# Kernel optimization log

Measured on AMD Instinct MI355X. Metric: run time of the kernel, lower is better.

## Reference

```python
import jax, jax.numpy as jnp
import numpy as np

FIRE_RATE = 0.5  # from init_kwargs
TOTAL_C = 16     # hidden_channels + 1


def _perception_filters(C, dtype):
    # Faithful to reg_perception_filters (including the sobel_x entries as written).
    identity = jnp.array([[0.0, 0.0, 0.0], [0.0, 1.0, 0.0], [0.0, 0.0, 0.0]], dtype=dtype)
    sobel_x = jnp.array([[1.0, 0.0, 1.0], [2.0, 0.0, -2.0], [1.0, 0.0, -1.0]], dtype=dtype) / 8.0
    sobel_y = jnp.array([[1.0, 2.0, 1.0], [0.0, 0.0, 0.0], [-1.0, -2.0, -1.0]], dtype=dtype) / 8.0
    f = jnp.stack([identity, sobel_x, sobel_y])[:, None, :, :]  # [3,1,3,3]
    # Grouped depthwise conv: each input channel -> 3 outputs, ordered
    # [ch0_id, ch0_sx, ch0_sy, ch1_id, ...] matching the torch per-channel cat.
    return jnp.tile(f, (C, 1, 1, 1))  # [3C,1,3,3]


def setup_inputs() -> dict:
    key = jax.random.key(0)
    k1, k2, k3, k4, k5, k6 = jax.random.split(key, 6)
    B, C, H, W = 32, TOTAL_C, 256, 256
    P = 3 * C  # perception channels = 48
    return {
        "grid": jax.random.normal(k1, (B, C, H, W), dtype=jnp.float32),
        "noise": jax.random.normal(k2, (B, 1, H, W), dtype=jnp.float32),
        "w1": jax.random.normal(k3, (128, P), dtype=jnp.float32) * 0.05,
        "b1": jax.random.normal(k4, (128,), dtype=jnp.float32) * 0.05,
        "w2": jax.random.normal(k5, (C, 128), dtype=jnp.float32) * 0.05,
        "b2": jax.random.normal(k6, (C,), dtype=jnp.float32) * 0.05,
    }


def reference(grid, noise, w1, b1, w2, b2):
    B, C, H, W = grid.shape
    filt = _perception_filters(C, grid.dtype)  # [3C,1,3,3]
    # Per-channel identity/sobel stencil as one grouped depthwise conv.
    perception = jax.lax.conv_general_dilated(
        grid, filt, window_strides=(1, 1), padding="SAME",
        dimension_numbers=("NCHW", "OIHW", "NCHW"), feature_group_count=C,
    )  # [B,3C,H,W]
    # update_net: 1x1 conv -> ReLU -> 1x1 conv (expressed as channel GEMMs)
    h = jax.nn.relu(jnp.einsum("oc,bchw->bohw", w1, perception) + b1[None, :, None, None])
    update = jnp.einsum("oc,bchw->bohw", w2, h) + b2[None, :, None, None]
    # stochastic mask: (randn < fire_rate), broadcast over channels
    mask = (noise < FIRE_RATE).astype(grid.dtype)
    return jnp.clip(grid + update * mask, -2.0, 2.0)
```

## Files before the change

kernel.cpp:

```cpp
#include <hip/hip_runtime.h>

#define NC   16
#define NP   48
#define NH   128
#define HDIM 256
#define WDIM 256
#define HW   (HDIM*WDIM)

#define PSTR  56
#define W1STR 56
#define W2STR 136
#define HSTR  136

typedef __attribute__((ext_vector_type(8))) short short8;
typedef __attribute__((ext_vector_type(4))) float f32x4;

__device__ __forceinline__ short f2bf(float f) {
    unsigned u = __float_as_uint(f);
    u += 0x7FFFu + ((u >> 16) & 1u);
    return (short)(u >> 16);
}

__global__ __launch_bounds__(256, 3) void nca_mfma_kernel(
    const float* __restrict__ grid,
    const float* __restrict__ noise,
    const float* __restrict__ w1,
    const float* __restrict__ b1,
    const float* __restrict__ w2,
    const float* __restrict__ b2,
    float* __restrict__ out)
{
    __shared__ short sP[HDIM * PSTR + 8];
    __shared__ union {
        struct { short w1[NH * W1STR + 8]; short w2[NC * W2STR]; } s;
        short H[4][16 * HSTR];
    } sU;

    const int tid = threadIdx.x;
    const int b = blockIdx.x >> 8;
    const int y = blockIdx.x & 255;

    {
        const int x = tid;
        const bool ym = (y > 0), yp = (y < HDIM - 1);
        const bool xm = (x > 0), xp = (x < WDIM - 1);
        const int xl = xm ? x - 1 : 0;
        const int xr = xp ? x + 1 : x;
        const size_t base = (size_t)b * NC * HW + (size_t)y * WDIM;

        float p[NP];
        #pragma unroll
        for (int c = 0; c < NC; ++c) {
            const float* rowM = grid + base + (size_t)c * HW;
            const float* rowT = rowM + (ym ? -WDIM : 0);
            const float* rowB = rowM + (yp ?  WDIM : 0);

            float tl0 = rowT[xl], tm0 = rowT[x], tr0 = rowT[xr];
            float ml0 = rowM[xl], mm  = rowM[x], mr0 = rowM[xr];
            float bl0 = rowB[xl], bm0 = rowB[x], br0 = rowB[xr];

            float tl = (ym && xm) ? tl0 : 0.f;
            float tm = ym         ? tm0 : 0.f;
            float tr = (ym && xp) ? tr0 : 0.f;
            float ml = xm         ? ml0 : 0.f;
            float mr = xp         ? mr0 : 0.f;
            float bl = (yp && xm) ? bl0 : 0.f;
            float bm = yp         ? bm0 : 0.f;
            float br = (yp && xp) ? br0 : 0.f;

            p[3*c]     = mm;
            p[3*c + 1] = (tl + tr + 2.f*ml - 2.f*mr + bl - br) * 0.125f;
            p[3*c + 2] = (tl + 2.f*tm + tr - bl - 2.f*bm - br) * 0.125f;
        }
        short* pw = &sP[x * PSTR];
        #pragma unroll
        for (int i = 0; i < 6; ++i) {
            short8 v;
            #pragma unroll
            for (int j = 0; j < 8; ++j) v[j] = f2bf(p[8*i + j]);
            *(short8*)&pw[8*i] = v;
        }
        short8 z = {};
        *(short8*)&pw[48] = z;
        if (tid == 0) *(short8*)&sP[HDIM * PSTR] = z;
    }

    {
        const int o = tid >> 1, half = tid & 1;
        const float* src = w1 + o * NP + half * 24;
        short* dst = &sU.s.w1[o * W1STR + half * 24];
        #pragma unroll
        for (int i = 0; i < 3; ++i) {
            short8 v;
            #pragma unroll
            for (int j = 0; j < 8; ++j) v[j] = f2bf(src[8*i + j]);
            *(short8*)&dst[8*i] = v;
        }
        if (half) { short8 z = {}; *(short8*)&sU.s.w1[o * W1STR + 48] = z; }
    }
    {
        const int j = tid >> 4, seg = tid & 15;
        const float* src = w2 + j * NH + seg * 8;
        short8 v;
        #pragma unroll
        for (int k = 0; k < 8; ++k) v[k] = f2bf(src[k]);
        *(short8*)&sU.s.w2[j * W2STR + seg * 8] = v;
    }
    __syncthreads();

    const int wv   = tid >> 6;
    const int lane = tid & 63;
    const int q    = lane >> 4;
    const int l15  = lane & 15;

    short8 w1f[8][2];
    #pragma unroll
    for (int n = 0; n < 8; ++n) {
        #pragma unroll
        for (int t = 0; t < 2; ++t) {
            const int kb = 32*t + 8*q;
            short8 v = *(const short8*)&sU.s.w1[(16*n + l15) * W1STR + kb];
            if (kb >= NP) { short8 z = {}; v = z; }
            w1f[n][t] = v;
        }
    }
    short8 w2f[4];
    #pragma unroll
    for (int t = 0; t < 4; ++t) {
        short8 v;
        #pragma unroll
        for (int jj = 0; jj < 8; ++jj) v[jj] = sU.s.w2[l15 * W2STR + jj*16 + 4*t + q];
        w2f[t] = v;
    }
    float b1v[8];
    #pragma unroll
    for (int n = 0; n < 8; ++n) b1v[n] = b1[16*n + l15];
    const float b2v = b2[l15];

    __syncthreads();

    short* Hb = sU.H[wv];
    #pragma unroll
    for (int mt = 0; mt < 4; ++mt) {
        const int px0 = (wv * 4 + mt) * 16;
        const short* pr = &sP[(px0 + l15) * PSTR];
        const short8 a0 = *(const short8*)&pr[8*q];
        short8 a1 = *(const short8*)&pr[32 + 8*q];
        if (q == 3) { short8 z = {}; a1 = z; }

        f32x4 acc[8];
        #pragma unroll
        for (int n = 0; n < 8; ++n) { f32x4 t4 = {b1v[n], b1v[n], b1v[n], b1v[n]}; acc[n] = t4; }
        #pragma unroll
        for (int n = 0; n < 8; ++n) {
            acc[n] = __builtin_amdgcn_mfma_f32_16x16x32_bf16(a0, w1f[n][0], acc[n], 0, 0, 0);
            acc[n] = __builtin_amdgcn_mfma_f32_16x16x32_bf16(a1, w1f[n][1], acc[n], 0, 0, 0);
        }
        #pragma unroll
        for (int r = 0; r < 4; ++r) {
            short8 hv;
            #pragma unroll
            for (int n = 0; n < 8; ++n) hv[n] = f2bf(fmaxf(acc[n][r], 0.f));
            *(short8*)&Hb[(q*4 + r) * HSTR + l15 * 8] = hv;
        }
        f32x4 acc2 = {b2v, b2v, b2v, b2v};
        #pragma unroll
        for (int t = 0; t < 4; ++t) {
            const short8 af = *(const short8*)&Hb[l15 * HSTR + 32*t + 8*q];
            acc2 = __builtin_amdgcn_mfma_f32_16x16x32_bf16(af, w2f[t], acc2, 0, 0, 0);
        }
        const int px = px0 + 4*q;
        const size_t gi = (size_t)b * NC * HW + (size_t)l15 * HW + (size_t)y * WDIM + px;
        const float4 g  = *(const float4*)&grid[gi];
        const float4 nz = *(const float4*)&noise[(size_t)b * HW + (size_t)y * WDIM + px];
        float4 o;
        o.x = fminf(fmaxf(g.x + acc2[0] * (nz.x < 0.5f ? 1.f : 0.f), -2.f), 2.f);
        o.y = fminf(fmaxf(g.y + acc2[1] * (nz.y < 0.5f ? 1.f : 0.f), -2.f), 2.f);
        o.z = fminf(fmaxf(g.z + acc2[2] * (nz.z < 0.5f ? 1.f : 0.f), -2.f), 2.f);
        o.w = fminf(fmaxf(g.w + acc2[3] * (nz.w < 0.5f ? 1.f : 0.f), -2.f), 2.f);
        *(float4*)&out[gi] = o;
    }
}

extern "C" void kernel_launch(void* const* d_in, const int* in_sizes, int n_in,
                              void* d_out, int out_size, void* d_ws, size_t ws_size,
                              hipStream_t stream) {
    const float* grid  = (const float*)d_in[0];
    const float* noise = (const float*)d_in[1];
    const float* w1    = (const float*)d_in[2];
    const float* b1    = (const float*)d_in[3];
    const float* w2    = (const float*)d_in[4];
    const float* b2    = (const float*)d_in[5];
    float* out = (float*)d_out;

    dim3 g(32 * 256);
    nca_mfma_kernel<<<g, 256, 0, stream>>>(grid, noise, w1, b1, w2, b2, out);
}
```

Before: 412.9 us.

## Stage stencil rows through LDS, keep W1 fragments in LDS, raise occupancy

Stencil inputs are now loaded cooperatively as three float4 rows per channel into shared memory, double-stepped with barriers, instead of nine scalar global loads per thread per channel. W1 fragments are kept pre-swizzled in LDS and read per MFMA rather than held in registers. The perception and H buffers now share one LDS region, and launch bounds are raised to 4 blocks per SM. Float-to-bf16 conversion uses the packed hardware instruction. The per-channel loop now has two barriers per channel, 32 in total, which adds synchronization overhead in exchange for fewer registers and less redundant global traffic.

```diff
diff --git a/kernel.cpp b/kernel.cpp
--- a/kernel.cpp
+++ b/kernel.cpp
@@ -7,21 +7,21 @@
 #define WDIM 256
 #define HW   (HDIM*WDIM)
 
-#define PSTR  56
-#define W1STR 56
+#define PSTR  48
+#define HSTR  136
 #define W2STR 136
-#define HSTR  136
 
 typedef __attribute__((ext_vector_type(8))) short short8;
 typedef __attribute__((ext_vector_type(4))) float f32x4;
-
-__device__ __forceinline__ short f2bf(float f) {
-    unsigned u = __float_as_uint(f);
-    u += 0x7FFFu + ((u >> 16) & 1u);
-    return (short)(u >> 16);
+typedef __attribute__((ext_vector_type(4))) int   int4v;
+
+__device__ __forceinline__ unsigned cvt_pk(float lo, float hi) {
+    unsigned r;
+    asm("v_cvt_pk_bf16_f32 %0, %1, %2" : "=v"(r) : "v"(lo), "v"(hi));
+    return r;
 }
 
-__global__ __launch_bounds__(256, 3) void nca_mfma_kernel(
+__global__ __launch_bounds__(256, 4) void nca_mfma_kernel(
     const float* __restrict__ grid,
     const float* __restrict__ noise,
     const float* __restrict__ w1,
@@ -30,106 +30,51 @@
     const float* __restrict__ b2,
     float* __restrict__ out)
 {
-    __shared__ short sP[HDIM * PSTR + 8];
-    __shared__ union {
-        struct { short w1[NH * W1STR + 8]; short w2[NC * W2STR]; } s;
-        short H[4][16 * HSTR];
-    } sU;
-
-    const int tid = threadIdx.x;
-    const int b = blockIdx.x >> 8;
-    const int y = blockIdx.x & 255;
-
-    {
-        const int x = tid;
-        const bool ym = (y > 0), yp = (y < HDIM - 1);
-        const bool xm = (x > 0), xp = (x < WDIM - 1);
-        const int xl = xm ? x - 1 : 0;
-        const int xr = xp ? x + 1 : x;
-        const size_t base = (size_t)b * NC * HW + (size_t)y * WDIM;
-
-        float p[NP];
-        #pragma unroll
-        for (int c = 0; c < NC; ++c) {
-            const float* rowM = grid + base + (size_t)c * HW;
-            const float* rowT = rowM + (ym ? -WDIM : 0);
-            const float* rowB = rowM + (yp ?  WDIM : 0);
-
-            float tl0 = rowT[xl], tm0 = rowT[x], tr0 = rowT[xr];
-            float ml0 = rowM[xl], mm  = rowM[x], mr0 = rowM[xr];
-            float bl0 = rowB[xl], bm0 = rowB[x], br0 = rowB[xr];
-
-            float tl = (ym && xm) ? tl0 : 0.f;
-            float tm = ym         ? tm0 : 0.f;
-            float tr = (ym && xp) ? tr0 : 0.f;
-            float ml = xm         ? ml0 : 0.f;
-            float mr = xp         ? mr0 : 0.f;
-            float bl = (yp && xm) ? bl0 : 0.f;
-            float bm = yp         ? bm0 : 0.f;
-            float br = (yp && xp) ? br0 : 0.f;
-
-            p[3*c]     = mm;
-            p[3*c + 1] = (tl + tr + 2.f*ml - 2.f*mr + bl - br) * 0.125f;
-            p[3*c + 2] = (tl + 2.f*tm + tr - bl - 2.f*bm - br) * 0.125f;
-        }
-        short* pw = &sP[x * PSTR];
-        #pragma unroll
-        for (int i = 0; i < 6; ++i) {
-            short8 v;
-            #pragma unroll
-            for (int j = 0; j < 8; ++j) v[j] = f2bf(p[8*i + j]);
-            *(short8*)&pw[8*i] = v;
-        }
-        short8 z = {};
-        *(short8*)&pw[48] = z;
-        if (tid == 0) *(short8*)&sP[HDIM * PSTR] = z;
-    }
-
-    {
-        const int o = tid >> 1, half = tid & 1;
-        const float* src = w1 + o * NP + half * 24;
-        short* dst = &sU.s.w1[o * W1STR + half * 24];
-        #pragma unroll
-        for (int i = 0; i < 3; ++i) {
-            short8 v;
-            #pragma unroll
-            for (int j = 0; j < 8; ++j) v[j] = f2bf(src[8*i + j]);
-            *(short8*)&dst[8*i] = v;
-        }
-        if (half) { short8 z = {}; *(short8*)&sU.s.w1[o * W1STR + 48] = z; }
-    }
-    {
-        const int j = tid >> 4, seg = tid & 15;
-        const float* src = w2 + j * NH + seg * 8;
-        short8 v;
-        #pragma unroll
-        for (int k = 0; k < 8; ++k) v[k] = f2bf(src[k]);
-        *(short8*)&sU.s.w2[j * W2STR + seg * 8] = v;
-    }
-    __syncthreads();
-
+    __shared__ short sW1F[8 * 768];
+    __shared__ short sP[HDIM * PSTR];
+
+    short* w2s = sP;
+    float* sS  = (float*)&sP[10736];
+
+    const int tid  = threadIdx.x;
+    const int b    = blockIdx.x >> 8;
+    const int y    = blockIdx.x & 255;
     const int wv   = tid >> 6;
     const int lane = tid & 63;
     const int q    = lane >> 4;
     const int l15  = lane & 15;
 
-    short8 w1f[8][2];
-    #pragma unroll
-    for (int n = 0; n < 8; ++n) {
-        #pragma unroll
-        for (int t = 0; t < 2; ++t) {
-            const int kb = 32*t + 8*q;
-            short8 v = *(const short8*)&sU.s.w1[(16*n + l15) * W1STR + kb];
-            if (kb >= NP) { short8 z = {}; v = z; }
-            w1f[n][t] = v;
-        }
-    }
+    {
+        const int o = tid >> 1, half = tid & 1;
+        const float* src = w1 + o * NP + 24 * half;
+        const int n = o >> 4, r15 = o & 15;
+        #pragma unroll
+        for (int g = 0; g < 3; ++g) {
+            const int k0 = 24 * half + 8 * g;
+            const int tt = k0 >> 5, qq = (k0 & 31) >> 3;
+            unsigned u0 = cvt_pk(src[8*g+0], src[8*g+1]);
+            unsigned u1 = cvt_pk(src[8*g+2], src[8*g+3]);
+            unsigned u2 = cvt_pk(src[8*g+4], src[8*g+5]);
+            unsigned u3 = cvt_pk(src[8*g+6], src[8*g+7]);
+            int4v v = {(int)u0, (int)u1, (int)u2, (int)u3};
+            *(int4v*)&sW1F[n*768 + (tt ? 512 : 0) + (qq*16 + r15)*8] = v;
+        }
+        const int j = tid >> 4, seg = tid & 15;
+        const float* s2 = w2 + j * NH + seg * 8;
+        unsigned v0 = cvt_pk(s2[0], s2[1]), v1 = cvt_pk(s2[2], s2[3]);
+        unsigned v2 = cvt_pk(s2[4], s2[5]), v3 = cvt_pk(s2[6], s2[7]);
+        int4v vv = {(int)v0, (int)v1, (int)v2, (int)v3};
+        *(int4v*)&w2s[j * W2STR + seg * 8] = vv;
+        if (tid < 3) { sS[tid*258 + 256] = 0.f; sS[tid*258 + 257] = 0.f; }
+    }
+    __syncthreads();
+
     short8 w2f[4];
     #pragma unroll
     for (int t = 0; t < 4; ++t) {
         short8 v;
         #pragma unroll
-        for (int jj = 0; jj < 8; ++jj) v[jj] = sU.s.w2[l15 * W2STR + jj*16 + 4*t + q];
+        for (int jj = 0; jj < 8; ++jj) v[jj] = w2s[l15 * W2STR + jj*16 + 4*t + q];
         w2f[t] = v;
     }
     float b1v[8];
@@ -137,31 +82,95 @@
     for (int n = 0; n < 8; ++n) b1v[n] = b1[16*n + l15];
     const float b2v = b2[l15];
 
+    const int  x   = tid;
+    const bool ld  = (tid < 192);
+    const int  r   = tid >> 6, seg = tid & 63;
+    int rowY = y - 1 + r; rowY = rowY < 0 ? 0 : (rowY > 255 ? 255 : rowY);
+    const bool zr = (r == 0 && y == 0) || (r == 2 && y == 255);
+    const float* gp = grid + (size_t)b * NC * HW + (size_t)rowY * WDIM + 4 * seg;
+
+    float4 v0 = {0.f, 0.f, 0.f, 0.f};
+    if (ld) { v0 = *(const float4*)gp; gp += HW; if (zr) { float4 z = {0,0,0,0}; v0 = z; } }
+    if (ld) *(float4*)&sS[r*258 + 4*seg] = v0;
     __syncthreads();
 
-    short* Hb = sU.H[wv];
+    const int xl = x ? (x - 1) : 256;
+    const int xr = (x < 255) ? (x + 1) : 256;
+
+    unsigned pk[24];
+    float carry = 0.f;
+    #pragma unroll
+    for (int c = 0; c < 16; ++c) {
+        float4 vn = {0.f, 0.f, 0.f, 0.f};
+        if (ld && c < 15) { vn = *(const float4*)gp; gp += HW; if (zr) { float4 z = {0,0,0,0}; vn = z; } }
+
+        const float tl = sS[xl],       tm = sS[x],       tr = sS[xr];
+        const float ml = sS[258 + xl], mm = sS[258 + x], mr = sS[258 + xr];
+        const float bl = sS[516 + xl], bm = sS[516 + x], br = sS[516 + xr];
+        const float p1 = (tl + tr + 2.f*ml - 2.f*mr + bl - br) * 0.125f;
+        const float p2 = (tl + 2.f*tm + tr - bl - 2.f*bm - br) * 0.125f;
+        if (c & 1) { pk[(3*c - 1) / 2] = cvt_pk(carry, mm); pk[(3*c + 1) / 2] = cvt_pk(p1, p2); }
+        else       { pk[3*c / 2]       = cvt_pk(mm, p1);    carry = p2; }
+
+        __syncthreads();
+        if (ld && c < 15) *(float4*)&sS[r*258 + 4*seg] = vn;
+        __syncthreads();
+    }
+
+    {
+        short* row = &sP[x * PSTR];
+        #pragma unroll
+        for (int i = 0; i < 6; ++i) {
+            int4v v = {(int)pk[4*i], (int)pk[4*i+1], (int)pk[4*i+2], (int)pk[4*i+3]};
+            *(int4v*)&row[8*i] = v;
+        }
+    }
+    __syncthreads();
+
+    short8 aF0[3], aF1[3];
+    #pragma unroll
+    for (int m = 1; m < 4; ++m) {
+        const short* pr = &sP[((wv*4 + m)*16 + l15) * PSTR];
+        aF0[m-1] = *(const short8*)&pr[8*q];
+        short8 a1 = {};
+        if (q < 2) a1 = *(const short8*)&pr[32 + 8*q];
+        aF1[m-1] = a1;
+    }
+    short* Hb = &sP[(wv*64 + 16) * PSTR];
+
     #pragma unroll
     for (int mt = 0; mt < 4; ++mt) {
-        const int px0 = (wv * 4 + mt) * 16;
-        const short* pr = &sP[(px0 + l15) * PSTR];
-        const short8 a0 = *(const short8*)&pr[8*q];
-        short8 a1 = *(const short8*)&pr[32 + 8*q];
-        if (q == 3) { short8 z = {}; a1 = z; }
+        short8 a0, a1;
+        if (mt == 0) {
+            const short* pr = &sP[(wv*64 + l15) * PSTR];
+            a0 = *(const short8*)&pr[8*q];
+            short8 z = {}; a1 = z;
+            if (q < 2) a1 = *(const short8*)&pr[32 + 8*q];
+        } else { a0 = aF0[mt-1]; a1 = aF1[mt-1]; }
 
         f32x4 acc[8];
         #pragma unroll
         for (int n = 0; n < 8; ++n) { f32x4 t4 = {b1v[n], b1v[n], b1v[n], b1v[n]}; acc[n] = t4; }
         #pragma unroll
         for (int n = 0; n < 8; ++n) {
-            acc[n] = __builtin_amdgcn_mfma_f32_16x16x32_bf16(a0, w1f[n][0], acc[n], 0, 0, 0);
-            acc[n] = __builtin_amdgcn_mfma_f32_16x16x32_bf16(a1, w1f[n][1], acc[n], 0, 0, 0);
-        }
-        #pragma unroll
-        for (int r = 0; r < 4; ++r) {
-            short8 hv;
-            #pragma unroll
-            for (int n = 0; n < 8; ++n) hv[n] = f2bf(fmaxf(acc[n][r], 0.f));
-            *(short8*)&Hb[(q*4 + r) * HSTR + l15 * 8] = hv;
+            const short8 bf0 = *(const short8*)&sW1F[n*768 + lane*8];
+            acc[n] = __builtin_amdgcn_mfma_f32_16x16x32_bf16(a0, bf0, acc[n], 0, 0, 0);
+        }
+        #pragma unroll
+        for (int n = 0; n < 8; ++n) {
+            short8 bf1 = {};
+            if (lane < 32) bf1 = *(const short8*)&sW1F[n*768 + 512 + lane*8];
+            acc[n] = __builtin_amdgcn_mfma_f32_16x16x32_bf16(a1, bf1, acc[n], 0, 0, 0);
+        }
+
+        #pragma unroll
+        for (int rr = 0; rr < 4; ++rr) {
+            unsigned h0 = cvt_pk(fmaxf(acc[0][rr], 0.f), fmaxf(acc[1][rr], 0.f));
+            unsigned h1 = cvt_pk(fmaxf(acc[2][rr], 0.f), fmaxf(acc[3][rr], 0.f));
+            unsigned h2 = cvt_pk(fmaxf(acc[4][rr], 0.f), fmaxf(acc[5][rr], 0.f));
+            unsigned h3 = cvt_pk(fmaxf(acc[6][rr], 0.f), fmaxf(acc[7][rr], 0.f));
+            int4v v = {(int)h0, (int)h1, (int)h2, (int)h3};
+            *(int4v*)&Hb[(q*4 + rr) * HSTR + l15 * 8] = v;
         }
         f32x4 acc2 = {b2v, b2v, b2v, b2v};
         #pragma unroll
@@ -169,7 +178,8 @@
             const short8 af = *(const short8*)&Hb[l15 * HSTR + 32*t + 8*q];
             acc2 = __builtin_amdgcn_mfma_f32_16x16x32_bf16(af, w2f[t], acc2, 0, 0, 0);
         }
-        const int px = px0 + 4*q;
+        const int px0 = (wv*4 + mt) * 16;
+        const int px  = px0 + 4*q;
         const size_t gi = (size_t)b * NC * HW + (size_t)l15 * HW + (size_t)y * WDIM + px;
         const float4 g  = *(const float4*)&grid[gi];
         const float4 nz = *(const float4*)&noise[(size_t)b * HW + (size_t)y * WDIM + px];
```

Result: slower. 449.0 us (+8.7%).
